# Optimization experiments

Measured on AMD Instinct MI355X. Metric: run time of the kernel, lower is better.

Reference implementation:

```python
import jax, jax.numpy as jnp
import numpy as np

B, S, D, H = 4, 2048, 1024, 16
HD = D // H  # head_dim = 64


def setup_inputs() -> dict:
    key = jax.random.key(0)
    ks = jax.random.split(key, 5)
    scale = 1.0 / np.sqrt(D)
    return {
        "x": jax.random.normal(ks[0], (B, S, D), dtype=jnp.float32),
        "Wq": jax.random.normal(ks[1], (D, D), dtype=jnp.float32) * scale,
        "Wk": jax.random.normal(ks[2], (D, D), dtype=jnp.float32) * scale,
        "Wv": jax.random.normal(ks[3], (D, D), dtype=jnp.float32) * scale,
        "Wo": jax.random.normal(ks[4], (D, D), dtype=jnp.float32) * scale,
        "bo": jnp.zeros((D,), dtype=jnp.float32),
    }


def reference(x, Wq, Wk, Wv, Wo, bo):
    b, n, d_in = x.shape
    # projections: [b, n, d_out] -> [b, h, n, hd]
    def heads(t):
        return t.reshape(b, n, H, HD).transpose(0, 2, 1, 3)
    q = heads(x @ Wq)
    k = heads(x @ Wk)
    v = heads(x @ Wv)
    # attention scores [b, h, n, n], causal mask, scaled softmax
    scores = jnp.einsum('bhqd,bhkd->bhqk', q, k)
    causal = jnp.tril(jnp.ones((n, n), dtype=bool))  # True = keep
    scores = jnp.where(causal, scores, -jnp.inf)
    weights = jax.nn.softmax(scores / np.sqrt(HD), axis=-1)
    # context: [b, h, n, hd] -> [b, n, d_out]
    ctx = jnp.einsum('bhqk,bhkd->bhqd', weights, v)
    ctx = ctx.transpose(0, 2, 1, 3).reshape(b, n, D)
    return ctx @ Wo + bo
```

## Files before the change

kernel.cpp:

```cpp
#include <hip/hip_runtime.h>

#define B_ 4
#define S_ 2048
#define D_ 1024
#define H_ 16
#define HD_ 64

typedef __bf16 bf16x8 __attribute__((ext_vector_type(8)));
typedef float f32x4 __attribute__((ext_vector_type(4)));
typedef float f32x16 __attribute__((ext_vector_type(16)));
typedef unsigned short u16;
typedef unsigned short u16x8 __attribute__((ext_vector_type(8)));

__device__ __forceinline__ u16 f2b(float f) {
  unsigned u = __builtin_bit_cast(unsigned, f);
  return (u16)((u + 0x7FFFu + ((u >> 16) & 1u)) >> 16);
}

__device__ __forceinline__ void gll16(const void* g, void* l) {
  __builtin_amdgcn_global_load_lds(
      (const __attribute__((address_space(1))) void*)g,
      (__attribute__((address_space(3))) void*)l, 16, 0, 0);
}

__device__ __forceinline__ f32x4 mfma16(bf16x8 a, bf16x8 b, f32x4 c) {
  return __builtin_amdgcn_mfma_f32_16x16x32_bf16(a, b, c, 0, 0, 0);
}
__device__ __forceinline__ f32x16 mfma32(bf16x8 a, bf16x8 b, f32x16 c) {
  return __builtin_amdgcn_mfma_f32_32x32x16_bf16(a, b, c, 0, 0, 0);
}

__device__ __forceinline__ unsigned cvtpk(float lo, float hi) {
  unsigned r;
  asm("v_cvt_pk_bf16_f32 %0, %1, %2" : "=v"(r) : "v"(lo), "v"(hi));
  return r;
}
__device__ __forceinline__ void plswap(unsigned& a, unsigned& b) {
  asm("v_permlane32_swap_b32 %0, %1" : "+v"(a), "+v"(b));
}
__device__ __forceinline__ bf16x8 mk8(unsigned a, unsigned b, unsigned c, unsigned d) {
  union { unsigned u[4]; bf16x8 v; } x;
  x.u[0] = a; x.u[1] = b; x.u[2] = c; x.u[3] = d;
  return x.v;
}

__global__ __launch_bounds__(256) void k_pre(
    const float* __restrict__ x, u16* __restrict__ xb,
    const float* __restrict__ Wq, const float* __restrict__ Wk,
    const float* __restrict__ Wv, const float* __restrict__ Wo,
    u16* __restrict__ wqkvt, u16* __restrict__ wot) {
  const int t = threadIdx.x;
  if (blockIdx.x < 8192) {
    int i = blockIdx.x * 256 + t;
    float4 f = reinterpret_cast<const float4*>(x)[i];
    ushort4 o;
    o.x = f2b(f.x); o.y = f2b(f.y); o.z = f2b(f.z); o.w = f2b(f.w);
    reinterpret_cast<ushort4*>(xb)[i] = o;
    return;
  }
  __shared__ float tile[32][33];
  const int id = blockIdx.x - 8192;
  const int z = id >> 10;
  const float* W;
  u16* Wt;
  if (z == 0)      { W = Wq; Wt = wqkvt; }
  else if (z == 1) { W = Wk; Wt = wqkvt + (size_t)D_ * D_; }
  else if (z == 2) { W = Wv; Wt = wqkvt + (size_t)2 * D_ * D_; }
  else             { W = Wo; Wt = wot; }
  const int bx = (id & 31) * 32, by = ((id >> 5) & 31) * 32;
  const int tx = t & 31, ty = t >> 5;
  #pragma unroll
  for (int i = ty; i < 32; i += 8)
    tile[i][tx] = W[(size_t)(by + i) * D_ + bx + tx];
  __syncthreads();
  #pragma unroll
  for (int i = ty; i < 32; i += 8)
    Wt[(size_t)(bx + i) * D_ + by + tx] = f2b(tile[tx][i]);
}

__global__ __launch_bounds__(512, 2) void k_gemm_qkv(
    const u16* __restrict__ A, const u16* __restrict__ Bt,
    u16* __restrict__ q, u16* __restrict__ kk, u16* __restrict__ v) {
  constexpr int K = D_;
  constexpr int NT = K / 64;
  __shared__ __align__(16) u16 lA[2 * 256 * 64];
  __shared__ __align__(16) u16 lB[2 * 256 * 64];
  const int cpx = 48;
  const int id = blockIdx.x;
  const int swz = (id & 7) * cpx + (id >> 3);
  const int bx = swz % 12, by = swz / 12;
  const int m0 = by * 256, n0 = bx * 256;
  const int t = threadIdx.x, lane = t & 63, w = t >> 6;
  const int wr = w >> 2, wc = w & 3;
  const int lr = lane & 15, lg = lane >> 4;
  const int l7 = lr & 7;
  const int wrlr = wr * 16 + lr, wclr = wc * 16 + lr;
  const int srow = t >> 3;
  const int sch = (t & 7) ^ (srow & 7);
  const u16* gAs = A + (size_t)(m0 + srow) * K + sch * 8;
  const u16* gBs = Bt + (size_t)(n0 + srow) * K + sch * 8;

  f32x4 acc[8][4] = {};
  bf16x8 Af[4][2], Bf0[2][2], Bf1[2][2];

  auto stageN = [&](int n) {
    if (n >= 4 * NT) return;
    const int kt2 = n >> 2, idx = n & 3;
    const int mat = idx & 1;
    const int h = (idx == 1 || idx == 2);
    const int bo = (kt2 & 1) * 16384;
    const u16* g = (mat ? gBs : gAs) + (size_t)(h * 128) * K + kt2 * 64;
    u16* l = (mat ? lB : lA) + bo + h * 8192 + t * 8;
    gll16(g, l);
    gll16(g + (size_t)64 * K, l + 4096);
  };

#define LOAD_A(qa_)                                                           \
  _Pragma("unroll") for (int il = 0; il < 4; ++il)                            \
  _Pragma("unroll") for (int ks = 0; ks < 2; ++ks)                            \
    Af[il][ks] = *(const bf16x8*)&lA[bufo + ((qa_)*128 + il * 32 + wrlr) * 64 +\
                                     (((ks * 4 + lg) ^ l7) * 8)];
#define LOAD_B(dst_, qb_)                                                     \
  _Pragma("unroll") for (int jl = 0; jl < 2; ++jl)                            \
  _Pragma("unroll") for (int ks = 0; ks < 2; ++ks)                            \
    dst_[jl][ks] = *(const bf16x8*)&lB[bufo + ((qb_)*128 + jl * 64 + wclr) * 64 +\
                                       (((ks * 4 + lg) ^ l7) * 8)];
#define MF(qa_, qb_, bf_)                                                     \
  __builtin_amdgcn_s_setprio(1);                                              \
  _Pragma("unroll") for (int il = 0; il < 4; ++il)                            \
  _Pragma("unroll") for (int jl = 0; jl < 2; ++jl)                            \
  _Pragma("unroll") for (int ks = 0; ks < 2; ++ks)                            \
    acc[(qa_)*4 + il][(qb_)*2 + jl] =                                         \
        mfma16(Af[il][ks], bf_[jl][ks], acc[(qa_)*4 + il][(qb_)*2 + jl]);     \
  __builtin_amdgcn_s_setprio(0);
#define BAR asm volatile("s_barrier" ::: "memory");
#define LGKM0 asm volatile("s_waitcnt lgkmcnt(0)" ::: "memory");

  stageN(0); stageN(1); stageN(3);
  stageN(2);
  stageN(4); stageN(5); stageN(7);

  for (int kt = 0; kt < NT; ++kt) {
    const int bufo = (kt & 1) * 16384;
    stageN(4 * (kt + 1) + 2);
    if (kt < NT - 1) {
      asm volatile("s_waitcnt vmcnt(8)" ::: "memory");
    } else {
      asm volatile("s_waitcnt vmcnt(0)" ::: "memory");
    }
    BAR
    LOAD_A(0) LOAD_B(Bf0, 0) LOAD_B(Bf1, 1)
    LGKM0
    MF(0, 0, Bf0) MF(0, 1, Bf1)
    BAR
    stageN(4 * (kt + 2) + 0);
    stageN(4 * (kt + 2) + 1);
    stageN(4 * (kt + 2) + 3);
    LOAD_A(1)
    LGKM0
    MF(1, 0, Bf0) MF(1, 1, Bf1)
    BAR
  }
#undef LOAD_A
#undef LOAD_B
#undef MF

  const int nclass = bx >> 2;
  const int b2 = m0 >> 11;
  const int s0b = m0 & 2047;
  const int h0 = (n0 & 1023) >> 6;
  if (nclass < 2) {
    u16* dst = nclass == 0 ? q : kk;
    const float sc = nclass == 0 ? 0.1803368801111f : 1.0f;
    #pragma unroll
    for (int i = 0; i < 8; ++i)
      #pragma unroll
      for (int j = 0; j < 4; ++j) {
        const size_t bh = (size_t)b2 * H_ + h0 + j;
        #pragma unroll
        for (int r = 0; r < 4; ++r) {
          int mloc = i * 32 + wr * 16 + lg * 4 + r;
          dst[(bh * S_ + s0b + mloc) * HD_ + wc * 16 + lr] =
              f2b(acc[i][j][r] * sc);
        }
      }
  } else {
    u16* vb = (u16*)lA;
    const int row = t >> 3, col0 = (t & 7) * 32;
    #pragma unroll
    for (int j = 0; j < 4; ++j) {
      __syncthreads();
      #pragma unroll
      for (int i = 0; i < 8; ++i)
        #pragma unroll
        for (int r = 0; r < 4; ++r)
          vb[(wc * 16 + lr) * 264 + i * 32 + wr * 16 + lg * 4 + r] =
              f2b(acc[i][j][r]);
      __syncthreads();
      u16* gv = v + ((size_t)(b2 * H_ + h0 + j) * HD_ + row) * S_ + s0b + col0;
      #pragma unroll
      for (int qq = 0; qq < 4; ++qq)
        *(u16x8*)(gv + qq * 8) = *(const u16x8*)&vb[row * 264 + col0 + qq * 8];
    }
  }
}

__global__ __launch_bounds__(512, 1) void k_gemm_proj2(
    const u16* __restrict__ A, const u16* __restrict__ Bt,
    const float* __restrict__ bias, float* __restrict__ out) {
  constexpr int K = D_;
  constexpr int NT = K / 64;
  __shared__ __align__(16) u16 lA[2 * 128 * 64];
  __shared__ __align__(16) u16 lB[2 * 256 * 64];
  const int cpx = 32;
  const int id = blockIdx.x;
  const int swz = (id & 7) * cpx + (id >> 3);
  const int bx = swz & 3, by = swz >> 2;
  const int m0 = by * 128, n0 = bx * 256;
  const int t = threadIdx.x, lane = t & 63, w = t >> 6;
  const int wr = w >> 2, wc = w & 3;
  const int lr = lane & 15, lg = lane >> 4;
  const int l7 = lr & 7;
  const int wrlr = wr * 16 + lr, wclr = wc * 16 + lr;
  const int srow = t >> 3;
  const int sch = (t & 7) ^ (srow & 7);
  const u16* gAs = A + (size_t)(m0 + srow) * K + sch * 8;
  const u16* gBs = Bt + (size_t)(n0 + srow) * K + sch * 8;

  f32x4 acc[4][4] = {};
  bf16x8 Af[2][2], Bf0[2][2], Bf1[2][2];

  auto stageN = [&](int n) {
    if (n >= 4 * NT) return;
    const int kt2 = n >> 2, idx = n & 3;
    const int koff = kt2 * 64;
    if (idx == 0) {
      gll16(gAs + koff, &lA[(kt2 & 1) * 8192 + t * 8]);
    } else if (idx == 2) {
      gll16(gAs + (size_t)64 * K + koff, &lA[(kt2 & 1) * 8192 + 4096 + t * 8]);
    } else if (idx == 1) {
      const u16* g = gBs + (size_t)128 * K + koff;
      u16* l = &lB[(kt2 & 1) * 16384 + 8192 + t * 8];
      gll16(g, l);
      gll16(g + (size_t)64 * K, l + 4096);
    } else {
      const u16* g = gBs + koff;
      u16* l = &lB[(kt2 & 1) * 16384 + t * 8];
      gll16(g, l);
      gll16(g + (size_t)64 * K, l + 4096);
    }
  };

#define LOAD_A(qa_)                                                           \
  _Pragma("unroll") for (int il = 0; il < 2; ++il)                            \
  _Pragma("unroll") for (int ks = 0; ks < 2; ++ks)                            \
    Af[il][ks] = *(const bf16x8*)&lA[bufoA + ((qa_)*64 + il * 32 + wrlr) * 64 +\
                                     (((ks * 4 + lg) ^ l7) * 8)];
#define LOAD_B(dst_, qb_)                                                     \
  _Pragma("unroll") for (int jl = 0; jl < 2; ++jl)                            \
  _Pragma("unroll") for (int ks = 0; ks < 2; ++ks)                            \
    dst_[jl][ks] = *(const bf16x8*)&lB[bufoB + ((qb_)*128 + jl * 64 + wclr) * 64 +\
                                       (((ks * 4 + lg) ^ l7) * 8)];
#define MF(qa_, qb_, bf_)                                                     \
  __builtin_amdgcn_s_setprio(1);                                              \
  _Pragma("unroll") for (int il = 0; il < 2; ++il)                            \
  _Pragma("unroll") for (int jl = 0; jl < 2; ++jl)                            \
  _Pragma("unroll") for (int ks = 0; ks < 2; ++ks)                            \
    acc[(qa_)*2 + il][(qb_)*2 + jl] =                                         \
        mfma16(Af[il][ks], bf_[jl][ks], acc[(qa_)*2 + il][(qb_)*2 + jl]);     \
  __builtin_amdgcn_s_setprio(0);

  stageN(0); stageN(1); stageN(3);
  stageN(2);
  stageN(4); stageN(5); stageN(7);

  for (int kt = 0; kt < NT; ++kt) {
    const int bufoA = (kt & 1) * 8192;
    const int bufoB = (kt & 1) * 16384;
    stageN(4 * (kt + 1) + 2);
    if (kt < NT - 1) {
      asm volatile("s_waitcnt vmcnt(6)" ::: "memory");
    } else {
      asm volatile("s_waitcnt vmcnt(0)" ::: "memory");
    }
    BAR
    LOAD_A(0) LOAD_B(Bf0, 0) LOAD_B(Bf1, 1)
    LGKM0
    MF(0, 0, Bf0) MF(0, 1, Bf1)
    BAR
    stageN(4 * (kt + 2) + 0);
    stageN(4 * (kt + 2) + 1);
    stageN(4 * (kt + 2) + 3);
    LOAD_A(1)
    LGKM0
    MF(1, 0, Bf0) MF(1, 1, Bf1)
    BAR
  }
#undef LOAD_A
#undef LOAD_B
#undef MF
#undef BAR
#undef LGKM0

  float bv[4];
  int nn[4];
  #pragma unroll
  for (int nj = 0; nj < 4; ++nj) {
    nn[nj] = n0 + (nj >> 1) * 128 + (nj & 1) * 64 + wc * 16 + lr;
    bv[nj] = bias[nn[nj]];
  }
  #pragma unroll
  for (int mi = 0; mi < 4; ++mi) {
    #pragma unroll
    for (int nj = 0; nj < 4; ++nj) {
      #pragma unroll
      for (int r = 0; r < 4; ++r) {
        int m = m0 + (mi >> 1) * 64 + (mi & 1) * 32 + wr * 16 + lg * 4 + r;
        out[(size_t)m * D_ + nn[nj]] = acc[mi][nj][r] + bv[nj];
      }
    }
  }
}

__global__ __launch_bounds__(256, 2) void k_attn(
    const u16* __restrict__ Qg, const u16* __restrict__ Kg,
    const u16* __restrict__ Vtg, u16* __restrict__ ctx) {
  __shared__ __align__(16) u16 Ks[2][64 * 64];
  __shared__ __align__(16) u16 Vs[2][64 * 64];
  const int ja = blockIdx.y, jb = 15 - ja, bh = blockIdx.x;
  const int t = threadIdx.x, l = t & 63, wq = t >> 6;
  const int lo5 = l & 31, hi = l >> 5, sw = l & 7;
  const size_t base = (size_t)bh * S_ * HD_;
  const int srow = t >> 3, sch = (t & 7) ^ (srow & 7);

  const int qw0A = ja * 128 + wq * 32, qw0B = jb * 128 + wq * 32;
  const int dktA = qw0A >> 6, dktB = qw0B >> 6;

  bf16x8 qA[4], qB[4];
  {
    const u16* qp = Qg + base + (size_t)(qw0A + lo5) * HD_ + hi * 8;
    #pragma unroll
    for (int di = 0; di < 4; ++di) qA[di] = *(const bf16x8*)(qp + di * 16);
    qp = Qg + base + (size_t)(qw0B + lo5) * HD_ + hi * 8;
    #pragma unroll
    for (int di = 0; di < 4; ++di) qB[di] = *(const bf16x8*)(qp + di * 16);
  }
  float mA = -1e30f, lsA = 0.f, mB = -1e30f, lsB = 0.f;
  f32x16 oA0 = {}, oA1 = {}, oB0 = {}, oB1 = {};

  auto stage = [&](int buf, int kb) {
    gll16(Kg + base + (size_t)(kb + srow) * HD_ + sch * 8, &Ks[buf][t * 8]);
    gll16(Kg + base + (size_t)(kb + 32 + srow) * HD_ + sch * 8, &Ks[buf][2048 + t * 8]);
    gll16(Vtg + base + (size_t)srow * S_ + kb + sch * 8, &Vs[buf][t * 8]);
    gll16(Vtg + base + (size_t)(32 + srow) * S_ + kb + sch * 8, &Vs[buf][2048 + t * 8]);
  };

  auto attend = [&](int buf, int kt, int qw0, int dkt, const bf16x8 (&qf)[4],
                    float& m_r, float& l_r, f32x16& o0, f32x16& o1) {
    const u16* KB = &Ks[buf][0];
    const u16* VB = &Vs[buf][0];
    f32x16 s0 = {}, s1 = {};
    #pragma unroll
    for (int di = 0; di < 4; ++di)
      s0 = mfma32(*(const bf16x8*)&KB[lo5 * 64 + (((di * 2 + hi) ^ sw) * 8)],
                  qf[di], s0);
    #pragma unroll
    for (int di = 0; di < 4; ++di)
      s1 = mfma32(*(const bf16x8*)&KB[(32 + lo5) * 64 + (((di * 2 + hi) ^ sw) * 8)],
                  qf[di], s1);
    if (kt == dkt) {
      int qrel = qw0 + lo5 - kt * 64;
      #pragma unroll
      for (int r = 0; r < 16; ++r) {
        int k0 = (r & 3) + 8 * (r >> 2) + 4 * hi;
        if (k0 > qrel) s0[r] = -1e30f;
        if (k0 + 32 > qrel) s1[r] = -1e30f;
      }
    }
    float tm = fmaxf(s0[0], s1[0]);
    #pragma unroll
    for (int r = 1; r < 16; ++r) tm = fmaxf(tm, fmaxf(s0[r], s1[r]));
    tm = fmaxf(tm, __shfl_xor(tm, 32));
    float mn = fmaxf(m_r, tm);
    float rescale = __builtin_amdgcn_exp2f(m_r - mn);
    m_r = mn;
    float sum = 0.f;
    #pragma unroll
    for (int r = 0; r < 16; ++r) { s0[r] = __builtin_amdgcn_exp2f(s0[r] - mn); sum += s0[r]; }
    #pragma unroll
    for (int r = 0; r < 16; ++r) { s1[r] = __builtin_amdgcn_exp2f(s1[r] - mn); sum += s1[r]; }
    sum += __shfl_xor(sum, 32);
    l_r = l_r * rescale + sum;
    o0 *= rescale;
    o1 *= rescale;
    unsigned a0 = cvtpk(s0[0], s0[1]), b0 = cvtpk(s0[4], s0[5]); plswap(a0, b0);
    unsigned a1 = cvtpk(s0[2], s0[3]), b1 = cvtpk(s0[6], s0[7]); plswap(a1, b1);
    unsigned a2 = cvtpk(s0[8], s0[9]), b2 = cvtpk(s0[12], s0[13]); plswap(a2, b2);
    unsigned a3 = cvtpk(s0[10], s0[11]), b3 = cvtpk(s0[14], s0[15]); plswap(a3, b3);
    bf16x8 p0 = mk8(a0, a1, b0, b1), p1 = mk8(a2, a3, b2, b3);
    a0 = cvtpk(s1[0], s1[1]); b0 = cvtpk(s1[4], s1[5]); plswap(a0, b0);
    a1 = cvtpk(s1[2], s1[3]); b1 = cvtpk(s1[6], s1[7]); plswap(a1, b1);
    a2 = cvtpk(s1[8], s1[9]); b2 = cvtpk(s1[12], s1[13]); plswap(a2, b2);
    a3 = cvtpk(s1[10], s1[11]); b3 = cvtpk(s1[14], s1[15]); plswap(a3, b3);
    bf16x8 p2 = mk8(a0, a1, b0, b1), p3 = mk8(a2, a3, b2, b3);
    o0 = mfma32(*(const bf16x8*)&VB[lo5 * 64 + (((0 + hi) ^ sw) * 8)], p0, o0);
    o0 = mfma32(*(const bf16x8*)&VB[lo5 * 64 + (((2 + hi) ^ sw) * 8)], p1, o0);
    o0 = mfma32(*(const bf16x8*)&VB[lo5 * 64 + (((4 + hi) ^ sw) * 8)], p2, o0);
    o0 = mfma32(*(const bf16x8*)&VB[lo5 * 64 + (((6 + hi) ^ sw) * 8)], p3, o0);
    o1 = mfma32(*(const bf16x8*)&VB[(32 + lo5) * 64 + (((0 + hi) ^ sw) * 8)], p0, o1);
    o1 = mfma32(*(const bf16x8*)&VB[(32 + lo5) * 64 + (((2 + hi) ^ sw) * 8)], p1, o1);
    o1 = mfma32(*(const bf16x8*)&VB[(32 + lo5) * 64 + (((4 + hi) ^ sw) * 8)], p2, o1);
    o1 = mfma32(*(const bf16x8*)&VB[(32 + lo5) * 64 + (((6 + hi) ^ sw) * 8)], p3, o1);
  };

  const int nt = 2 * jb + 2;
  stage(0, 0);
  __syncthreads();
  int cur = 0;
  for (int kt = 0; kt < nt; ++kt) {
    if (kt + 1 < nt) stage(cur ^ 1, (kt + 1) * 64);
    if (kt <= dktA) attend(cur, kt, qw0A, dktA, qA, mA, lsA, oA0, oA1);
    if (kt <= dktB) attend(cur, kt, qw0B, dktB, qB, mB, lsB, oB0, oB1);
    __syncthreads();
    cur ^= 1;
  }

  const int b = bh >> 4, h = bh & 15;
  {
    float inv = 1.f / lsA;
    u16* cp = ctx + ((size_t)b * S_ + qw0A + lo5) * D_ + h * 64 + hi * 4;
    #pragma unroll
    for (int rg = 0; rg < 4; ++rg) {
      ushort4 o4;
      o4.x = f2b(oA0[rg * 4 + 0] * inv); o4.y = f2b(oA0[rg * 4 + 1] * inv);
      o4.z = f2b(oA0[rg * 4 + 2] * inv); o4.w = f2b(oA0[rg * 4 + 3] * inv);
      *(ushort4*)(cp + rg * 8) = o4;
      o4.x = f2b(oA1[rg * 4 + 0] * inv); o4.y = f2b(oA1[rg * 4 + 1] * inv);
      o4.z = f2b(oA1[rg * 4 + 2] * inv); o4.w = f2b(oA1[rg * 4 + 3] * inv);
      *(ushort4*)(cp + 32 + rg * 8) = o4;
    }
  }
  {
    float inv = 1.f / lsB;
    u16* cp = ctx + ((size_t)b * S_ + qw0B + lo5) * D_ + h * 64 + hi * 4;
    #pragma unroll
    for (int rg = 0; rg < 4; ++rg) {
      ushort4 o4;
      o4.x = f2b(oB0[rg * 4 + 0] * inv); o4.y = f2b(oB0[rg * 4 + 1] * inv);
      o4.z = f2b(oB0[rg * 4 + 2] * inv); o4.w = f2b(oB0[rg * 4 + 3] * inv);
      *(ushort4*)(cp + rg * 8) = o4;
      o4.x = f2b(oB1[rg * 4 + 0] * inv); o4.y = f2b(oB1[rg * 4 + 1] * inv);
      o4.z = f2b(oB1[rg * 4 + 2] * inv); o4.w = f2b(oB1[rg * 4 + 3] * inv);
      *(ushort4*)(cp + 32 + rg * 8) = o4;
    }
  }
}

extern "C" void kernel_launch(void* const* d_in, const int* in_sizes, int n_in,
                              void* d_out, int out_size, void* d_ws, size_t ws_size,
                              hipStream_t stream) {
  const float* x  = (const float*)d_in[0];
  const float* Wq = (const float*)d_in[1];
  const float* Wk = (const float*)d_in[2];
  const float* Wv = (const float*)d_in[3];
  const float* Wo = (const float*)d_in[4];
  const float* bo = (const float*)d_in[5];
  float* out = (float*)d_out;
  (void)in_sizes; (void)n_in; (void)out_size; (void)ws_size;

  char* p = (char*)d_ws;
  const size_t NTOK = (size_t)B_ * S_;
  u16* xb    = (u16*)p; p += NTOK * D_ * 2;
  u16* wqkvt = (u16*)p; p += (size_t)3 * D_ * D_ * 2;
  u16* wot   = (u16*)p; p += (size_t)D_ * D_ * 2;
  u16* Qg    = (u16*)p; p += NTOK * D_ * 2;
  u16* Kg    = (u16*)p; p += NTOK * D_ * 2;
  u16* Vtg   = (u16*)p; p += NTOK * D_ * 2;
  u16* ctx   = (u16*)p; p += NTOK * D_ * 2;

  k_pre<<<dim3(8192 + 4096), dim3(256), 0, stream>>>(x, xb, Wq, Wk, Wv, Wo,
                                                     wqkvt, wot);
  k_gemm_qkv<<<dim3(384), dim3(512), 0, stream>>>(xb, wqkvt, Qg, Kg, Vtg);
  k_attn<<<dim3(B_ * H_, 8), dim3(256), 0, stream>>>(Qg, Kg, Vtg, ctx);
  k_gemm_proj2<<<dim3(256), dim3(512), 0, stream>>>(ctx, wot, bo, out);
}
```

Measured before the change: 176.3 us.

## Split fused QKV GEMM into separate QK and V GEMM kernels

Replaces the single 384-block QKV projection kernel with a 256-block kernel for Q/K (256x256 tiles) and a separate 256-block kernel for V using 128x256 tiles with a transposed store. The aim is to remove the wave-quantization tail of 384 large tiles on the GPU's compute units and to give the V transpose epilogue a smaller per-block footprint. The cost is an extra kernel launch and a V GEMM with smaller tiles, which means less operand reuse. It also moves BAR/LGKM0 macro definitions so the new kernel can use them.

```diff
diff --git a/kernel.cpp b/kernel.cpp
--- a/kernel.cpp
+++ b/kernel.cpp
@@ -78,17 +78,17 @@
     Wt[(size_t)(bx + i) * D_ + by + tx] = f2b(tile[tx][i]);
 }
 
-__global__ __launch_bounds__(512, 2) void k_gemm_qkv(
+__global__ __launch_bounds__(512, 2) void k_gemm_qk(
     const u16* __restrict__ A, const u16* __restrict__ Bt,
-    u16* __restrict__ q, u16* __restrict__ kk, u16* __restrict__ v) {
+    u16* __restrict__ q, u16* __restrict__ kk) {
   constexpr int K = D_;
   constexpr int NT = K / 64;
   __shared__ __align__(16) u16 lA[2 * 256 * 64];
   __shared__ __align__(16) u16 lB[2 * 256 * 64];
-  const int cpx = 48;
+  const int cpx = 32;
   const int id = blockIdx.x;
   const int swz = (id & 7) * cpx + (id >> 3);
-  const int bx = swz % 12, by = swz / 12;
+  const int bx = swz & 7, by = swz >> 3;
   const int m0 = by * 256, n0 = bx * 256;
   const int t = threadIdx.x, lane = t & 63, w = t >> 6;
   const int wr = w >> 2, wc = w & 3;
@@ -169,39 +169,137 @@
   const int b2 = m0 >> 11;
   const int s0b = m0 & 2047;
   const int h0 = (n0 & 1023) >> 6;
-  if (nclass < 2) {
-    u16* dst = nclass == 0 ? q : kk;
-    const float sc = nclass == 0 ? 0.1803368801111f : 1.0f;
-    #pragma unroll
-    for (int i = 0; i < 8; ++i)
+  u16* dst = nclass == 0 ? q : kk;
+  const float sc = nclass == 0 ? 0.1803368801111f : 1.0f;
+  #pragma unroll
+  for (int i = 0; i < 8; ++i)
+    #pragma unroll
+    for (int j = 0; j < 4; ++j) {
+      const size_t bh = (size_t)b2 * H_ + h0 + j;
       #pragma unroll
-      for (int j = 0; j < 4; ++j) {
-        const size_t bh = (size_t)b2 * H_ + h0 + j;
-        #pragma unroll
-        for (int r = 0; r < 4; ++r) {
-          int mloc = i * 32 + wr * 16 + lg * 4 + r;
-          dst[(bh * S_ + s0b + mloc) * HD_ + wc * 16 + lr] =
-              f2b(acc[i][j][r] * sc);
-        }
+      for (int r = 0; r < 4; ++r) {
+        int mloc = i * 32 + wr * 16 + lg * 4 + r;
+        dst[(bh * S_ + s0b + mloc) * HD_ + wc * 16 + lr] =
+            f2b(acc[i][j][r] * sc);
       }
-  } else {
-    u16* vb = (u16*)lA;
-    const int row = t >> 3, col0 = (t & 7) * 32;
-    #pragma unroll
-    for (int j = 0; j < 4; ++j) {
-      __syncthreads();
+    }
+}
+
+__global__ __launch_bounds__(512, 1) void k_gemm_v(
+    const u16* __restrict__ A, const u16* __restrict__ Bt,
+    u16* __restrict__ v) {
+  constexpr int K = D_;
+  constexpr int NT = K / 64;
+  __shared__ __align__(16) u16 lA[2 * 128 * 64];
+  __shared__ __align__(16) u16 lB[2 * 256 * 64];
+  const int cpx = 32;
+  const int id = blockIdx.x;
+  const int swz = (id & 7) * cpx + (id >> 3);
+  const int bx = swz & 3, by = swz >> 2;
+  const int m0 = by * 128, n0 = bx * 256;
+  const int t = threadIdx.x, lane = t & 63, w = t >> 6;
+  const int wr = w >> 2, wc = w & 3;
+  const int lr = lane & 15, lg = lane >> 4;
+  const int l7 = lr & 7;
+  const int wrlr = wr * 16 + lr, wclr = wc * 16 + lr;
+  const int srow = t >> 3;
+  const int sch = (t & 7) ^ (srow & 7);
+  const u16* gAs = A + (size_t)(m0 + srow) * K + sch * 8;
+  const u16* gBs = Bt + (size_t)(n0 + srow) * K + sch * 8;
+
+  f32x4 acc[4][4] = {};
+  bf16x8 Af[2][2], Bf0[2][2], Bf1[2][2];
+
+  auto stageN = [&](int n) {
+    if (n >= 4 * NT) return;
+    const int kt2 = n >> 2, idx = n & 3;
+    const int koff = kt2 * 64;
+    if (idx == 0) {
+      gll16(gAs + koff, &lA[(kt2 & 1) * 8192 + t * 8]);
+    } else if (idx == 2) {
+      gll16(gAs + (size_t)64 * K + koff, &lA[(kt2 & 1) * 8192 + 4096 + t * 8]);
+    } else if (idx == 1) {
+      const u16* g = gBs + (size_t)128 * K + koff;
+      u16* l = &lB[(kt2 & 1) * 16384 + 8192 + t * 8];
+      gll16(g, l);
+      gll16(g + (size_t)64 * K, l + 4096);
+    } else {
+      const u16* g = gBs + koff;
+      u16* l = &lB[(kt2 & 1) * 16384 + t * 8];
+      gll16(g, l);
+      gll16(g + (size_t)64 * K, l + 4096);
+    }
+  };
+
+#define LOAD_A(qa_)                                                           \
+  _Pragma("unroll") for (int il = 0; il < 2; ++il)                            \
+  _Pragma("unroll") for (int ks = 0; ks < 2; ++ks)                            \
+    Af[il][ks] = *(const bf16x8*)&lA[bufoA + ((qa_)*64 + il * 32 + wrlr) * 64 +\
+                                     (((ks * 4 + lg) ^ l7) * 8)];
+#define LOAD_B(dst_, qb_)                                                     \
+  _Pragma("unroll") for (int jl = 0; jl < 2; ++jl)                            \
+  _Pragma("unroll") for (int ks = 0; ks < 2; ++ks)                            \
+    dst_[jl][ks] = *(const bf16x8*)&lB[bufoB + ((qb_)*128 + jl * 64 + wclr) * 64 +\
+                                       (((ks * 4 + lg) ^ l7) * 8)];
+#define MF(qa_, qb_, bf_)                                                     \
+  __builtin_amdgcn_s_setprio(1);                                              \
+  _Pragma("unroll") for (int il = 0; il < 2; ++il)                            \
+  _Pragma("unroll") for (int jl = 0; jl < 2; ++jl)                            \
+  _Pragma("unroll") for (int ks = 0; ks < 2; ++ks)                            \
+    acc[(qa_)*2 + il][(qb_)*2 + jl] =                                         \
+        mfma16(Af[il][ks], bf_[jl][ks], acc[(qa_)*2 + il][(qb_)*2 + jl]);     \
+  __builtin_amdgcn_s_setprio(0);
+
+  stageN(0); stageN(1); stageN(3);
+  stageN(2);
+  stageN(4); stageN(5); stageN(7);
+
+  for (int kt = 0; kt < NT; ++kt) {
+    const int bufoA = (kt & 1) * 8192;
+    const int bufoB = (kt & 1) * 16384;
+    stageN(4 * (kt + 1) + 2);
+    if (kt < NT - 1) {
+      asm volatile("s_waitcnt vmcnt(6)" ::: "memory");
+    } else {
+      asm volatile("s_waitcnt vmcnt(0)" ::: "memory");
+    }
+    BAR
+    LOAD_A(0) LOAD_B(Bf0, 0) LOAD_B(Bf1, 1)
+    LGKM0
+    MF(0, 0, Bf0) MF(0, 1, Bf1)
+    BAR
+    stageN(4 * (kt + 2) + 0);
+    stageN(4 * (kt + 2) + 1);
+    stageN(4 * (kt + 2) + 3);
+    LOAD_A(1)
+    LGKM0
+    MF(1, 0, Bf0) MF(1, 1, Bf1)
+    BAR
+  }
+#undef LOAD_A
+#undef LOAD_B
+#undef MF
+#undef BAR
+#undef LGKM0
+
+  const int b2 = m0 >> 11;
+  const int s0b = m0 & 2047;
+  const int h0 = n0 >> 6;
+  u16* vb = (u16*)lA;
+  const int row = t >> 3, col0 = (t & 7) * 16;
+  #pragma unroll
+  for (int nj = 0; nj < 4; ++nj) {
+    __syncthreads();
+    #pragma unroll
+    for (int mi = 0; mi < 4; ++mi)
       #pragma unroll
-      for (int i = 0; i < 8; ++i)
-        #pragma unroll
-        for (int r = 0; r < 4; ++r)
-          vb[(wc * 16 + lr) * 264 + i * 32 + wr * 16 + lg * 4 + r] =
-              f2b(acc[i][j][r]);
-      __syncthreads();
-      u16* gv = v + ((size_t)(b2 * H_ + h0 + j) * HD_ + row) * S_ + s0b + col0;
-      #pragma unroll
-      for (int qq = 0; qq < 4; ++qq)
-        *(u16x8*)(gv + qq * 8) = *(const u16x8*)&vb[row * 264 + col0 + qq * 8];
-    }
+      for (int r = 0; r < 4; ++r)
+        vb[(wc * 16 + lr) * 136 + mi * 32 + wr * 16 + lg * 4 + r] =
+            f2b(acc[mi][nj][r]);
+    __syncthreads();
+    u16* gv = v + ((size_t)(b2 * H_ + h0 + nj) * HD_ + row) * S_ + s0b + col0;
+    *(u16x8*)(gv) = *(const u16x8*)&vb[row * 136 + col0];
+    *(u16x8*)(gv + 8) = *(const u16x8*)&vb[row * 136 + col0 + 8];
   }
 }
 
@@ -269,6 +367,8 @@
     acc[(qa_)*2 + il][(qb_)*2 + jl] =                                         \
         mfma16(Af[il][ks], bf_[jl][ks], acc[(qa_)*2 + il][(qb_)*2 + jl]);     \
   __builtin_amdgcn_s_setprio(0);
+#define BAR asm volatile("s_barrier" ::: "memory");
+#define LGKM0 asm volatile("s_waitcnt lgkmcnt(0)" ::: "memory");
 
   stageN(0); stageN(1); stageN(3);
   stageN(2);
@@ -480,7 +580,9 @@
 
   k_pre<<<dim3(8192 + 4096), dim3(256), 0, stream>>>(x, xb, Wq, Wk, Wv, Wo,
                                                      wqkvt, wot);
-  k_gemm_qkv<<<dim3(384), dim3(512), 0, stream>>>(xb, wqkvt, Qg, Kg, Vtg);
+  k_gemm_qk<<<dim3(256), dim3(512), 0, stream>>>(xb, wqkvt, Qg, Kg);
+  k_gemm_v<<<dim3(256), dim3(512), 0, stream>>>(
+      xb, wqkvt + (size_t)2 * D_ * D_, Vtg);
   k_attn<<<dim3(B_ * H_, 8), dim3(256), 0, stream>>>(Qg, Kg, Vtg, ctx);
   k_gemm_proj2<<<dim3(256), dim3(512), 0, stream>>>(ctx, wot, bo, out);
 }
```

Result: no change. 173.2 us (-1.7%).
